# Performance work log

Hardware: AMD Instinct MI355X
Metric: run time of the kernel (lower is better)

## Reference

```python
import jax, jax.numpy as jnp
import numpy as np

B, T, V, H, L = 4, 2048, 32000, 512, 2

def setup_inputs() -> dict:
    key = jax.random.key(0)
    ks = jax.random.split(key, 8)
    s = 0.04  # ~1/sqrt(H) scaling to keep tanh unsaturated
    return {
        "x": jax.random.randint(ks[0], (B, T), 0, V, dtype=jnp.int32),
        "embed": jax.random.normal(ks[1], (V, H), jnp.float32) * s,
        "W_ih": jax.random.normal(ks[2], (L, H, H), jnp.float32) * s,
        "b_ih": jax.random.normal(ks[3], (L, H), jnp.float32) * s,
        "W_hh": jax.random.normal(ks[4], (L, H, H), jnp.float32) * s,
        "b_hh": jax.random.normal(ks[5], (L, H), jnp.float32) * s,
        "W_out": jax.random.normal(ks[6], (V, H), jnp.float32) * s,
        "b_out": jax.random.normal(ks[7], (V,), jnp.float32) * s,
    }

def reference(x, embed, W_ih, b_ih, W_hh, b_hh, W_out, b_out):
    emb = embed[x]                      # [B, T, H]
    num_layers = W_ih.shape[0]
    Bsz = x.shape[0]
    Hd = embed.shape[1]

    def step(h, x_t):                   # h: [L, B, H], x_t: [B, H]
        inp = x_t
        new_h = []
        for l in range(num_layers):     # small fixed layer count
            hl = jnp.tanh(inp @ W_ih[l].T + b_ih[l] + h[l] @ W_hh[l].T + b_hh[l])
            new_h.append(hl)
            inp = hl
        out = inp @ W_out.T + b_out     # [B, V]
        return jnp.stack(new_h), out

    h0 = jnp.zeros((num_layers, Bsz, Hd), emb.dtype)
    h_final, outs = jax.lax.scan(step, h0, jnp.swapaxes(emb, 0, 1))  # outs: [T, B, V]
    return jnp.swapaxes(outs, 0, 1), h_final
```

## Files before the change

### kernel.cpp

```cpp
#include <hip/hip_runtime.h>
#include <stdint.h>

#define Bdim 4
#define Tdim 2048
#define Vdim 32000
#define Hdim 512
#define MROWS (Bdim * Tdim)

typedef unsigned short u16;
typedef __bf16 bf16x8 __attribute__((ext_vector_type(8)));
typedef float f32x4 __attribute__((ext_vector_type(4)));

__device__ __forceinline__ u16 f2bf(float f) {
  union { float f; uint32_t u; } a; a.f = f;
  uint32_t r = a.u + 0x7FFFu + ((a.u >> 16) & 1u);
  return (u16)(r >> 16);
}

__global__ void k_gather(const int* __restrict__ x, const float* __restrict__ embed,
                         u16* __restrict__ E) {
  int idx = blockIdx.x * 256 + threadIdx.x;
  int row = idx >> 7;
  int c4  = (idx & 127) << 2;
  int tok = x[row];
  const float4 v = *(const float4*)(embed + (size_t)tok * Hdim + c4);
  *(ushort4*)(E + (size_t)row * Hdim + c4) =
      make_ushort4(f2bf(v.x), f2bf(v.y), f2bf(v.z), f2bf(v.w));
}

__global__ void k_f2b(const float* __restrict__ in, u16* __restrict__ out, int n4) {
  int idx = blockIdx.x * 256 + threadIdx.x;
  if (idx >= n4) return;
  const float4 v = *(const float4*)(in + (size_t)idx * 4);
  *(ushort4*)(out + (size_t)idx * 4) =
      make_ushort4(f2bf(v.x), f2bf(v.y), f2bf(v.z), f2bf(v.w));
}

__device__ __forceinline__ void g2l16(const void* g, void* l) {
  __builtin_amdgcn_global_load_lds(
      (const __attribute__((address_space(1))) uint32_t*)g,
      (__attribute__((address_space(3))) uint32_t*)l, 16, 0, 0);
}

__global__ __launch_bounds__(256, 2) void k_gemm(
    const u16* __restrict__ A, const u16* __restrict__ Bw, float* __restrict__ C,
    const float* __restrict__ bias1, const float* __restrict__ bias2,
    int M, int N, int K, int ntN)
{
  __shared__ u16 Al[128 * 64];
  __shared__ u16 Bl[128 * 64];
  const int bid = blockIdx.x;
  const int mt = bid / ntN, nt = bid % ntN;
  const int m0 = mt << 7, n0 = nt << 7;
  const int tid = threadIdx.x;
  const int l = tid & 63, w = tid >> 6;
  const int wy = w >> 1, wx = w & 1;
  const int frow = l & 15, fk = (l >> 4) << 3;

  f32x4 acc[4][4];
  #pragma unroll
  for (int a = 0; a < 4; ++a)
    #pragma unroll
    for (int b = 0; b < 4; ++b) acc[a][b] = f32x4{0.f, 0.f, 0.f, 0.f};

  for (int kb = 0; kb < K; kb += 64) {
    __syncthreads();
    #pragma unroll
    for (int is = 0; is < 4; ++is) {
      const int off = tid * 16 + is * 4096;
      const int lrow = off >> 7, lcolB = off & 127;
      g2l16(A  + (size_t)(m0 + lrow) * K + kb + (lcolB >> 1), (char*)Al + off);
      g2l16(Bw + (size_t)(n0 + lrow) * K + kb + (lcolB >> 1), (char*)Bl + off);
    }
    __syncthreads();
    #pragma unroll
    for (int ks = 0; ks < 2; ++ks) {
      bf16x8 af[4], bfr[4];
      #pragma unroll
      for (int mi = 0; mi < 4; ++mi)
        af[mi] = *(const bf16x8*)&Al[((wy * 64 + mi * 16 + frow) << 6) + ks * 32 + fk];
      #pragma unroll
      for (int ni = 0; ni < 4; ++ni)
        bfr[ni] = *(const bf16x8*)&Bl[((wx * 64 + ni * 16 + frow) << 6) + ks * 32 + fk];
      #pragma unroll
      for (int mi = 0; mi < 4; ++mi)
        #pragma unroll
        for (int ni = 0; ni < 4; ++ni)
          acc[mi][ni] = __builtin_amdgcn_mfma_f32_16x16x32_bf16(af[mi], bfr[ni], acc[mi][ni], 0, 0, 0);
    }
  }
  #pragma unroll
  for (int ni = 0; ni < 4; ++ni) {
    const int col = n0 + wx * 64 + ni * 16 + (l & 15);
    float bv = bias1[col];
    if (bias2) bv += bias2[col];
    #pragma unroll
    for (int mi = 0; mi < 4; ++mi) {
      const int row = m0 + wy * 64 + mi * 16 + ((l >> 4) << 2);
      #pragma unroll
      for (int r = 0; r < 4; ++r)
        C[(size_t)(row + r) * N + col] = acc[mi][ni][r] + bv;
    }
  }
}

#define SENT 0xFFFFFFFFu

__device__ __forceinline__ uint64_t al64(const uint64_t* p) {
  return __hip_atomic_load(p, __ATOMIC_RELAXED, __HIP_MEMORY_SCOPE_AGENT);
}
__device__ __forceinline__ void astore(uint32_t* p, uint32_t v) {
  __hip_atomic_store(p, v, __ATOMIC_RELAXED, __HIP_MEMORY_SCOPE_AGENT);
}
__device__ __forceinline__ bool bad2(uint64_t x) {
  return ((uint32_t)x == SENT) || ((uint32_t)(x >> 32) == SENT);
}
#define SPIN2(va, vb, P)                                          \
  while (bad2(va) || bad2(vb)) {                                  \
    if (bad2(va)) va = al64(P);                                   \
    if (bad2(vb)) vb = al64((P) + 1);                             \
  }

#define ROWDW 264

template <bool IS_L1>
__device__ __forceinline__ void scan_wg(
    const float* __restrict__ X0,
    const float* __restrict__ W1,
    const float* __restrict__ W2,
    const float* __restrict__ bi1, const float* __restrict__ bi2,
    uint32_t* __restrict__ H0b, uint32_t* __restrict__ H1b,
    float* __restrict__ hfin, int wgs, uint32_t* hsA, uint32_t* hsB)
{
  constexpr int NB = IS_L1 ? 32 : 16;
  const int tid = threadIdx.x;
  const int wv  = tid >> 6;
  const int l   = tid & 63;
  const int n   = l & 15;
  const int cq  = l >> 4;
  const int ng  = wgs * 64 + wv * 16 + n;
  const int fb  = n & 3;
  const int pb  = wv;
  const int q   = l;

  bf16x8 bw[NB];
  #pragma unroll
  for (int j = 0; j < NB; ++j) {
    const float* wrow;
    int koff;
    if constexpr (IS_L1) {
      if (j < 16) { wrow = W1 + (size_t)ng * Hdim; koff = j * 32; }
      else        { wrow = W2 + (size_t)ng * Hdim; koff = (j - 16) * 32; }
    } else        { wrow = W1 + (size_t)ng * Hdim; koff = j * 32; }
    const float4 a = *(const float4*)(wrow + koff + cq * 8);
    const float4 b = *(const float4*)(wrow + koff + cq * 8 + 4);
    bw[j][0] = (__bf16)a.x; bw[j][1] = (__bf16)a.y;
    bw[j][2] = (__bf16)a.z; bw[j][3] = (__bf16)a.w;
    bw[j][4] = (__bf16)b.x; bw[j][5] = (__bf16)b.y;
    bw[j][6] = (__bf16)b.z; bw[j][7] = (__bf16)b.w;
  }
  float bias = 0.f;
  if constexpr (IS_L1) bias = bi1[ng] + bi2[ng];

  const uint64_t *PpA = nullptr, *PpB = nullptr;
  uint64_t vaA = 0, vbA = 0, vaB = 0, vbB = 0;
  if constexpr (IS_L1) {
    PpA = (const uint64_t*)(H0b + ((size_t)pb * Tdim + 0) * 256 + 4 * q);
    vaA = al64(PpA); vbA = al64(PpA + 1);
  }

  #pragma unroll 1
  for (int t = 0; t < Tdim; ++t) {
    uint32_t* sA = hsA + (t & 1) * (4 * ROWDW);
    f32x4 ac[4];
    #pragma unroll
    for (int x = 0; x < 4; ++x) ac[x] = f32x4{0.f, 0.f, 0.f, 0.f};

    if constexpr (!IS_L1) {
      float x0v[4];
      #pragma unroll
      for (int r = 0; r < 4; ++r)
        x0v[r] = X0[((size_t)r * Tdim + t) * Hdim + ng];

      if (t > 0) {
        SPIN2(vaA, vbA, PpA);
        uint4 u;
        u.x = (uint32_t)vaA; u.y = (uint32_t)(vaA >> 32);
        u.z = (uint32_t)vbA; u.w = (uint32_t)(vbA >> 32);
        *(uint4*)(sA + pb * ROWDW + 4 * q) = u;
      }
      PpA = (const uint64_t*)(H0b + ((size_t)pb * Tdim + t) * 256 + 4 * q);
      vaA = al64(PpA); vbA = al64(PpA + 1);

      if (t > 0) {
        __syncthreads();
        const u16* sA16 = (const u16*)sA;
        #pragma unroll
        for (int j = 0; j < 16; ++j) {
          const bf16x8 af = *(const bf16x8*)&sA16[fb * (2 * ROWDW) + j * 32 + cq * 8];
          ac[j & 3] = __builtin_amdgcn_mfma_f32_16x16x32_bf16(af, bw[j], ac[j & 3], 0, 0, 0);
        }
      }
      const f32x4 s = (ac[0] + ac[1]) + (ac[2] + ac[3]);
      float hv[4], hp[4];
      #pragma unroll
      for (int r = 0; r < 4; ++r) hv[r] = tanhf(s[r] + x0v[r]);
      #pragma unroll
      for (int r = 0; r < 4; ++r) hp[r] = __shfl_xor(hv[r], 1);
      if (cq == 0) {
        if (!(n & 1)) {
          #pragma unroll
          for (int r = 0; r < 4; ++r) {
            const uint32_t wd = (uint32_t)f2bf(hv[r]) | ((uint32_t)f2bf(hp[r]) << 16);
            astore(&H0b[((size_t)r * Tdim + t) * 256 + (ng >> 1)], wd);
          }
        }
        if (t == Tdim - 1) {
          #pragma unroll
          for (int r = 0; r < 4; ++r) hfin[r * Hdim + ng] = hv[r];
        }
      }
    } else {
      uint32_t* sB = hsB + (t & 1) * (4 * ROWDW);
      if (t > 0) {
        SPIN2(vaB, vbB, PpB);
        uint4 u;
        u.x = (uint32_t)vaB; u.y = (uint32_t)(vaB >> 32);
        u.z = (uint32_t)vbB; u.w = (uint32_t)(vbB >> 32);
        *(uint4*)(sB + pb * ROWDW + 4 * q) = u;
        __syncthreads();
        const u16* sB16 = (const u16*)sB;
        #pragma unroll
        for (int j = 16; j < 32; ++j) {
          const bf16x8 af = *(const bf16x8*)&sB16[fb * (2 * ROWDW) + (j - 16) * 32 + cq * 8];
          ac[j & 3] = __builtin_amdgcn_mfma_f32_16x16x32_bf16(af, bw[j], ac[j & 3], 0, 0, 0);
        }
      }
      SPIN2(vaA, vbA, PpA);
      {
        uint4 u;
        u.x = (uint32_t)vaA; u.y = (uint32_t)(vaA >> 32);
        u.z = (uint32_t)vbA; u.w = (uint32_t)(vbA >> 32);
        *(uint4*)(sA + pb * ROWDW + 4 * q) = u;
      }
      {
        const int tn = (t + 1 < Tdim) ? t + 1 : t;
        PpA = (const uint64_t*)(H0b + ((size_t)pb * Tdim + tn) * 256 + 4 * q);
        vaA = al64(PpA); vbA = al64(PpA + 1);
      }
      __syncthreads();
      const u16* sA16 = (const u16*)sA;
      #pragma unroll
      for (int j = 0; j < 16; ++j) {
        const bf16x8 af = *(const bf16x8*)&sA16[fb * (2 * ROWDW) + j * 32 + cq * 8];
        ac[j & 3] = __builtin_amdgcn_mfma_f32_16x16x32_bf16(af, bw[j], ac[j & 3], 0, 0, 0);
      }
      const f32x4 s = (ac[0] + ac[1]) + (ac[2] + ac[3]);
      float hv[4], hp[4];
      #pragma unroll
      for (int r = 0; r < 4; ++r) hv[r] = tanhf(s[r] + bias);
      #pragma unroll
      for (int r = 0; r < 4; ++r) hp[r] = __shfl_xor(hv[r], 1);
      if (cq == 0) {
        if (!(n & 1)) {
          #pragma unroll
          for (int r = 0; r < 4; ++r) {
            const uint32_t wd = (uint32_t)f2bf(hv[r]) | ((uint32_t)f2bf(hp[r]) << 16);
            astore(&H1b[((size_t)r * Tdim + t) * 256 + (ng >> 1)], wd);
          }
        }
        if (t == Tdim - 1) {
          #pragma unroll
          for (int r = 0; r < 4; ++r) hfin[Bdim * Hdim + r * Hdim + ng] = hv[r];
        }
      }
      PpB = (const uint64_t*)(H1b + ((size_t)pb * Tdim + t) * 256 + 4 * q);
      vaB = al64(PpB); vbB = al64(PpB + 1);
    }
  }
}

__global__ __launch_bounds__(256, 1) void k_scan(
    const float* __restrict__ X0, const float* __restrict__ W_ih,
    const float* __restrict__ W_hh, const float* __restrict__ b_ih,
    const float* __restrict__ b_hh, uint32_t* __restrict__ H0b,
    uint32_t* __restrict__ H1b, float* __restrict__ hfin)
{
  __shared__ __align__(16) uint32_t hsA[2 * 4 * ROWDW];
  __shared__ __align__(16) uint32_t hsB[2 * 4 * ROWDW];
  const int blk = blockIdx.x;
  if (blk < 8)
    scan_wg<false>(X0, W_hh, nullptr, nullptr, nullptr, H0b, H1b, hfin, blk, hsA, hsB);
  else
    scan_wg<true>(nullptr, W_ih + Hdim * Hdim, W_hh + Hdim * Hdim,
                  b_ih + Hdim, b_hh + Hdim, H0b, H1b, hfin, blk - 8, hsA, hsB);
}

extern "C" void kernel_launch(void* const* d_in, const int* in_sizes, int n_in,
                              void* d_out, int out_size, void* d_ws, size_t ws_size,
                              hipStream_t stream)
{
  const int*   x     = (const int*)d_in[0];
  const float* embed = (const float*)d_in[1];
  const float* W_ih  = (const float*)d_in[2];
  const float* b_ih  = (const float*)d_in[3];
  const float* W_hh  = (const float*)d_in[4];
  const float* b_hh  = (const float*)d_in[5];
  const float* W_out = (const float*)d_in[6];
  const float* b_out = (const float*)d_in[7];
  float* out = (float*)d_out;

  char* ws = (char*)d_ws;
  u16* E       = (u16*)ws;
  u16* Wih0b   = E + (size_t)MROWS * Hdim;
  u16* Woutb   = Wih0b + Hdim * Hdim;
  float* X0    = (float*)(Woutb + (size_t)Vdim * Hdim);
  uint32_t* H0b = (uint32_t*)(X0 + (size_t)MROWS * Hdim);
  uint32_t* H1b = H0b + (size_t)MROWS * (Hdim / 2);

  k_gather<<<MROWS * (Hdim / 4) / 256, 256, 0, stream>>>(x, embed, E);
  k_f2b<<<(Hdim * Hdim / 4) / 256, 256, 0, stream>>>(W_ih, Wih0b, Hdim * Hdim / 4);
  k_f2b<<<(Vdim * Hdim / 4) / 256, 256, 0, stream>>>(W_out, Woutb, Vdim * Hdim / 4);

  k_gemm<<<(MROWS / 128) * (Hdim / 128), 256, 0, stream>>>(
      E, Wih0b, X0, b_ih, b_hh, MROWS, Hdim, Hdim, Hdim / 128);

  hipMemsetAsync(H0b, 0xFF, (size_t)MROWS * (Hdim / 2) * 4, stream);
  hipMemsetAsync(H1b, 0xFF, (size_t)MROWS * (Hdim / 2) * 4, stream);

  float* hfin = out + (size_t)MROWS * Vdim;
  k_scan<<<16, 256, 0, stream>>>(X0, W_ih, W_hh, b_ih, b_hh, H0b, H1b, hfin);

  k_gemm<<<(MROWS / 128) * (Vdim / 128), 256, 0, stream>>>(
      (const u16*)H1b, Woutb, out, b_out, nullptr, MROWS, Vdim, Hdim, Vdim / 128);
}
```

Baseline: 6.846 ms.

## Replace block-wide barrier with per-wave polling and staging in recurrent scan

Each wave now polls the whole previous hidden-state row itself, using wide cache-bypassing dwordx4 loads, and stages it into its own private LDS region, so the per-step __syncthreads is gone. Layer 1 issues its layer-0 load early and overlaps it with the recurrent MFMA work. Layer 0 is throttled so it stays no more than 128 steps ahead of layer 1. The scan grid grows to 128 blocks with only every eighth block active, which appears meant to spread the 16 workers across different XCDs or CUs. The cost is redundant global polling by every wave, plus reliance on inline asm ordering and cache-modifier semantics.

```diff
diff --git a/kernel.cpp b/kernel.cpp
--- a/kernel.cpp
+++ b/kernel.cpp
@@ -10,6 +10,7 @@
 typedef unsigned short u16;
 typedef __bf16 bf16x8 __attribute__((ext_vector_type(8)));
 typedef float f32x4 __attribute__((ext_vector_type(4)));
+typedef uint32_t u32x4 __attribute__((ext_vector_type(4)));
 
 __device__ __forceinline__ u16 f2bf(float f) {
   union { float f; uint32_t u; } a; a.f = f;
@@ -106,22 +107,96 @@
 
 #define SENT 0xFFFFFFFFu
 
-__device__ __forceinline__ uint64_t al64(const uint64_t* p) {
-  return __hip_atomic_load(p, __ATOMIC_RELAXED, __HIP_MEMORY_SCOPE_AGENT);
-}
 __device__ __forceinline__ void astore(uint32_t* p, uint32_t v) {
   __hip_atomic_store(p, v, __ATOMIC_RELAXED, __HIP_MEMORY_SCOPE_AGENT);
 }
-__device__ __forceinline__ bool bad2(uint64_t x) {
-  return ((uint32_t)x == SENT) || ((uint32_t)(x >> 32) == SENT);
-}
-#define SPIN2(va, vb, P)                                          \
-  while (bad2(va) || bad2(vb)) {                                  \
-    if (bad2(va)) va = al64(P);                                   \
-    if (bad2(vb)) vb = al64((P) + 1);                             \
-  }
-
-#define ROWDW 264
+__device__ __forceinline__ uint32_t aload(const uint32_t* p) {
+  return __hip_atomic_load(p, __ATOMIC_RELAXED, __HIP_MEMORY_SCOPE_AGENT);
+}
+
+__device__ __forceinline__ void pollload(const uint32_t* p, u32x4& a, u32x4& b,
+                                         u32x4& c, u32x4& d) {
+  asm volatile(
+      "global_load_dwordx4 %0, %4, off sc0\n\t"
+      "global_load_dwordx4 %1, %4, off offset:16 sc0\n\t"
+      "global_load_dwordx4 %2, %4, off offset:32 sc0\n\t"
+      "global_load_dwordx4 %3, %4, off offset:48 sc0\n\t"
+      "s_waitcnt vmcnt(0)"
+      : "=&v"(a), "=&v"(b), "=&v"(c), "=&v"(d)
+      : "v"(p) : "memory");
+  __builtin_amdgcn_sched_barrier(0);
+}
+__device__ __forceinline__ void pissue(const uint32_t* p, u32x4& a, u32x4& b,
+                                       u32x4& c, u32x4& d) {
+  asm volatile(
+      "global_load_dwordx4 %0, %4, off sc0\n\t"
+      "global_load_dwordx4 %1, %4, off offset:16 sc0\n\t"
+      "global_load_dwordx4 %2, %4, off offset:32 sc0\n\t"
+      "global_load_dwordx4 %3, %4, off offset:48 sc0"
+      : "=&v"(a), "=&v"(b), "=&v"(c), "=&v"(d)
+      : "v"(p) : "memory");
+}
+__device__ __forceinline__ void pwait(u32x4& a, u32x4& b, u32x4& c, u32x4& d) {
+  asm volatile("s_waitcnt vmcnt(0)"
+               : "+v"(a), "+v"(b), "+v"(c), "+v"(d) :: "memory");
+  __builtin_amdgcn_sched_barrier(0);
+}
+__device__ __forceinline__ bool any_sent(const u32x4& a, const u32x4& b,
+                                         const u32x4& c, const u32x4& d) {
+  bool bad = false;
+  #pragma unroll
+  for (int j = 0; j < 4; ++j)
+    bad |= (a[j] == SENT) | (b[j] == SENT) | (c[j] == SENT) | (d[j] == SENT);
+  return bad;
+}
+__device__ __forceinline__ void respin(const uint32_t* p, u32x4& a, u32x4& b,
+                                       u32x4& c, u32x4& d) {
+  int tr = 0;
+  while (any_sent(a, b, c, d)) {
+    if (tr < 2) {
+      pollload(p, a, b, c, d);
+    } else {
+      #pragma unroll
+      for (int j = 0; j < 4; ++j) {
+        if (a[j] == SENT) a[j] = aload(p + j);
+        if (b[j] == SENT) b[j] = aload(p + 4 + j);
+        if (c[j] == SENT) c[j] = aload(p + 8 + j);
+        if (d[j] == SENT) d[j] = aload(p + 12 + j);
+      }
+    }
+    ++tr;
+  }
+}
+__device__ __forceinline__ void spin16(const uint32_t* p, u32x4& a, u32x4& b,
+                                       u32x4& c, u32x4& d) {
+  pollload(p, a, b, c, d);
+  respin(p, a, b, c, d);
+}
+__device__ __forceinline__ void spin_word(const uint32_t* p) {
+  uint32_t v;
+  asm volatile("global_load_dword %0, %1, off sc0\n\ts_waitcnt vmcnt(0)"
+               : "=&v"(v) : "v"(p) : "memory");
+  __builtin_amdgcn_sched_barrier(0);
+  int tr = 0;
+  while (v == SENT) {
+    if (tr < 2)
+      asm volatile("global_load_dword %0, %1, off sc0\n\ts_waitcnt vmcnt(0)"
+                   : "=&v"(v) : "v"(p) : "memory");
+    else
+      v = aload(p);
+    ++tr;
+  }
+  __builtin_amdgcn_sched_barrier(0);
+}
+__device__ __forceinline__ void lds_guard() {
+  asm volatile("s_waitcnt lgkmcnt(0)" ::: "memory");
+  __builtin_amdgcn_sched_barrier(0);
+}
+
+#define STAGE(base, A, B, C, D) do {                      \
+    uint32_t* _d = (base) + sb * 264 + sq * 16;           \
+    *(u32x4*)(_d)      = (A); *(u32x4*)(_d + 4)  = (B);   \
+    *(u32x4*)(_d + 8)  = (C); *(u32x4*)(_d + 12) = (D); } while (0)
 
 template <bool IS_L1>
 __device__ __forceinline__ void scan_wg(
@@ -130,7 +205,7 @@
     const float* __restrict__ W2,
     const float* __restrict__ bi1, const float* __restrict__ bi2,
     uint32_t* __restrict__ H0b, uint32_t* __restrict__ H1b,
-    float* __restrict__ hfin, int wgs, uint32_t* hsA, uint32_t* hsB)
+    float* __restrict__ hfin, int wgs, uint32_t* hs)
 {
   constexpr int NB = IS_L1 ? 32 : 16;
   const int tid = threadIdx.x;
@@ -140,8 +215,13 @@
   const int cq  = l >> 4;
   const int ng  = wgs * 64 + wv * 16 + n;
   const int fb  = n & 3;
-  const int pb  = wv;
-  const int q   = l;
+  const int sb  = l >> 4;
+  const int sq  = l & 15;
+
+  uint32_t* hsA = hs + wv * 1056;
+  uint32_t* hsB = hs + 4224 + wv * 1056;
+  const u16* sA16 = (const u16*)hsA;
+  const u16* sB16 = (const u16*)hsB;
 
   bf16x8 bw[NB];
   #pragma unroll
@@ -162,120 +242,90 @@
   float bias = 0.f;
   if constexpr (IS_L1) bias = bi1[ng] + bi2[ng];
 
-  const uint64_t *PpA = nullptr, *PpB = nullptr;
-  uint64_t vaA = 0, vbA = 0, vaB = 0, vbB = 0;
-  if constexpr (IS_L1) {
-    PpA = (const uint64_t*)(H0b + ((size_t)pb * Tdim + 0) * 256 + 4 * q);
-    vaA = al64(PpA); vbA = al64(PpA + 1);
-  }
+  uint32_t* const Hout = IS_L1 ? H1b : H0b;
 
   #pragma unroll 1
   for (int t = 0; t < Tdim; ++t) {
-    uint32_t* sA = hsA + (t & 1) * (4 * ROWDW);
     f32x4 ac[4];
     #pragma unroll
-    for (int x = 0; x < 4; ++x) ac[x] = f32x4{0.f, 0.f, 0.f, 0.f};
+    for (int q = 0; q < 4; ++q) ac[q] = f32x4{0.f, 0.f, 0.f, 0.f};
+    float hv[4], hp[4];
 
     if constexpr (!IS_L1) {
+      u32x4 a, b, c, d;
+      if (t > 0)
+        spin16(H0b + ((size_t)sb * Tdim + (t - 1)) * 256 + sq * 16, a, b, c, d);
       float x0v[4];
       #pragma unroll
       for (int r = 0; r < 4; ++r)
         x0v[r] = X0[((size_t)r * Tdim + t) * Hdim + ng];
-
       if (t > 0) {
-        SPIN2(vaA, vbA, PpA);
-        uint4 u;
-        u.x = (uint32_t)vaA; u.y = (uint32_t)(vaA >> 32);
-        u.z = (uint32_t)vbA; u.w = (uint32_t)(vbA >> 32);
-        *(uint4*)(sA + pb * ROWDW + 4 * q) = u;
-      }
-      PpA = (const uint64_t*)(H0b + ((size_t)pb * Tdim + t) * 256 + 4 * q);
-      vaA = al64(PpA); vbA = al64(PpA + 1);
-
-      if (t > 0) {
-        __syncthreads();
-        const u16* sA16 = (const u16*)sA;
+        lds_guard();
+        STAGE(hsA, a, b, c, d);
         #pragma unroll
         for (int j = 0; j < 16; ++j) {
-          const bf16x8 af = *(const bf16x8*)&sA16[fb * (2 * ROWDW) + j * 32 + cq * 8];
+          const bf16x8 af = *(const bf16x8*)&sA16[fb * 528 + j * 32 + cq * 8];
           ac[j & 3] = __builtin_amdgcn_mfma_f32_16x16x32_bf16(af, bw[j], ac[j & 3], 0, 0, 0);
         }
       }
       const f32x4 s = (ac[0] + ac[1]) + (ac[2] + ac[3]);
-      float hv[4], hp[4];
       #pragma unroll
       for (int r = 0; r < 4; ++r) hv[r] = tanhf(s[r] + x0v[r]);
       #pragma unroll
       for (int r = 0; r < 4; ++r) hp[r] = __shfl_xor(hv[r], 1);
-      if (cq == 0) {
-        if (!(n & 1)) {
-          #pragma unroll
-          for (int r = 0; r < 4; ++r) {
-            const uint32_t wd = (uint32_t)f2bf(hv[r]) | ((uint32_t)f2bf(hp[r]) << 16);
-            astore(&H0b[((size_t)r * Tdim + t) * 256 + (ng >> 1)], wd);
-          }
+      if (cq == 0 && !(n & 1)) {
+        #pragma unroll
+        for (int r = 0; r < 4; ++r) {
+          const uint32_t wd = (uint32_t)f2bf(hv[r]) | ((uint32_t)f2bf(hp[r]) << 16);
+          astore(&Hout[((size_t)r * Tdim + t) * 256 + (ng >> 1)], wd);
         }
-        if (t == Tdim - 1) {
-          #pragma unroll
-          for (int r = 0; r < 4; ++r) hfin[r * Hdim + ng] = hv[r];
+      }
+      if (cq == 0 && t == Tdim - 1) {
+        #pragma unroll
+        for (int r = 0; r < 4; ++r) hfin[r * Hdim + ng] = hv[r];
+      }
+      if (t >= 128 && (t & 15) == 0)
+        spin_word(H1b + (size_t)(t - 128) * 256);
+    } else {
+      u32x4 a, b, c, d, e, f, g, h2;
+      if (t > 0) {
+        spin16(H1b + ((size_t)sb * Tdim + (t - 1)) * 256 + sq * 16, e, f, g, h2);
+        lds_guard();
+        STAGE(hsB, e, f, g, h2);
+        pissue(H0b + ((size_t)sb * Tdim + t) * 256 + sq * 16, a, b, c, d);
+        #pragma unroll
+        for (int j = 0; j < 16; ++j) {
+          const bf16x8 af = *(const bf16x8*)&sB16[fb * 528 + j * 32 + cq * 8];
+          ac[j & 3] = __builtin_amdgcn_mfma_f32_16x16x32_bf16(af, bw[16 + j], ac[j & 3], 0, 0, 0);
         }
-      }
-    } else {
-      uint32_t* sB = hsB + (t & 1) * (4 * ROWDW);
-      if (t > 0) {
-        SPIN2(vaB, vbB, PpB);
-        uint4 u;
-        u.x = (uint32_t)vaB; u.y = (uint32_t)(vaB >> 32);
-        u.z = (uint32_t)vbB; u.w = (uint32_t)(vbB >> 32);
-        *(uint4*)(sB + pb * ROWDW + 4 * q) = u;
-        __syncthreads();
-        const u16* sB16 = (const u16*)sB;
-        #pragma unroll
-        for (int j = 16; j < 32; ++j) {
-          const bf16x8 af = *(const bf16x8*)&sB16[fb * (2 * ROWDW) + (j - 16) * 32 + cq * 8];
-          ac[j & 3] = __builtin_amdgcn_mfma_f32_16x16x32_bf16(af, bw[j], ac[j & 3], 0, 0, 0);
+        pwait(a, b, c, d);
+        respin(H0b + ((size_t)sb * Tdim + t) * 256 + sq * 16, a, b, c, d);
+      } else {
+        spin16(H0b + ((size_t)sb * Tdim + 0) * 256 + sq * 16, a, b, c, d);
+      }
+      lds_guard();
+      STAGE(hsA, a, b, c, d);
+      #pragma unroll
+      for (int j = 0; j < 16; ++j) {
+        const bf16x8 af = *(const bf16x8*)&sA16[fb * 528 + j * 32 + cq * 8];
+        ac[j & 3] = __builtin_amdgcn_mfma_f32_16x16x32_bf16(af, bw[j], ac[j & 3], 0, 0, 0);
+      }
+      const f32x4 s = (ac[0] + ac[1]) + (ac[2] + ac[3]);
+      #pragma unroll
+      for (int r = 0; r < 4; ++r) hv[r] = tanhf(s[r] + bias);
+      #pragma unroll
+      for (int r = 0; r < 4; ++r) hp[r] = __shfl_xor(hv[r], 1);
+      if (cq == 0 && !(n & 1)) {
+        #pragma unroll
+        for (int r = 0; r < 4; ++r) {
+          const uint32_t wd = (uint32_t)f2bf(hv[r]) | ((uint32_t)f2bf(hp[r]) << 16);
+          astore(&Hout[((size_t)r * Tdim + t) * 256 + (ng >> 1)], wd);
         }
       }
-      SPIN2(vaA, vbA, PpA);
-      {
-        uint4 u;
-        u.x = (uint32_t)vaA; u.y = (uint32_t)(vaA >> 32);
-        u.z = (uint32_t)vbA; u.w = (uint32_t)(vbA >> 32);
-        *(uint4*)(sA + pb * ROWDW + 4 * q) = u;
-      }
-      {
-        const int tn = (t + 1 < Tdim) ? t + 1 : t;
-        PpA = (const uint64_t*)(H0b + ((size_t)pb * Tdim + tn) * 256 + 4 * q);
-        vaA = al64(PpA); vbA = al64(PpA + 1);
-      }
-      __syncthreads();
-      const u16* sA16 = (const u16*)sA;
-      #pragma unroll
-      for (int j = 0; j < 16; ++j) {
-        const bf16x8 af = *(const bf16x8*)&sA16[fb * (2 * ROWDW) + j * 32 + cq * 8];
-        ac[j & 3] = __builtin_amdgcn_mfma_f32_16x16x32_bf16(af, bw[j], ac[j & 3], 0, 0, 0);
-      }
-      const f32x4 s = (ac[0] + ac[1]) + (ac[2] + ac[3]);
-      float hv[4], hp[4];
-      #pragma unroll
-      for (int r = 0; r < 4; ++r) hv[r] = tanhf(s[r] + bias);
-      #pragma unroll
-      for (int r = 0; r < 4; ++r) hp[r] = __shfl_xor(hv[r], 1);
-      if (cq == 0) {
-        if (!(n & 1)) {
-          #pragma unroll
-          for (int r = 0; r < 4; ++r) {
-            const uint32_t wd = (uint32_t)f2bf(hv[r]) | ((uint32_t)f2bf(hp[r]) << 16);
-            astore(&H1b[((size_t)r * Tdim + t) * 256 + (ng >> 1)], wd);
-          }
-        }
-        if (t == Tdim - 1) {
-          #pragma unroll
-          for (int r = 0; r < 4; ++r) hfin[Bdim * Hdim + r * Hdim + ng] = hv[r];
-        }
-      }
-      PpB = (const uint64_t*)(H1b + ((size_t)pb * Tdim + t) * 256 + 4 * q);
-      vaB = al64(PpB); vbB = al64(PpB + 1);
+      if (cq == 0 && t == Tdim - 1) {
+        #pragma unroll
+        for (int r = 0; r < 4; ++r) hfin[Bdim * Hdim + r * Hdim + ng] = hv[r];
+      }
     }
   }
 }
@@ -286,14 +336,14 @@
     const float* __restrict__ b_hh, uint32_t* __restrict__ H0b,
     uint32_t* __restrict__ H1b, float* __restrict__ hfin)
 {
-  __shared__ __align__(16) uint32_t hsA[2 * 4 * ROWDW];
-  __shared__ __align__(16) uint32_t hsB[2 * 4 * ROWDW];
-  const int blk = blockIdx.x;
-  if (blk < 8)
-    scan_wg<false>(X0, W_hh, nullptr, nullptr, nullptr, H0b, H1b, hfin, blk, hsA, hsB);
+  __shared__ __align__(16) uint32_t hs[8448];
+  if (blockIdx.x & 7) return;
+  const int wg = blockIdx.x >> 3;
+  if (wg < 8)
+    scan_wg<false>(X0, W_hh, nullptr, nullptr, nullptr, H0b, H1b, hfin, wg, hs);
   else
     scan_wg<true>(nullptr, W_ih + Hdim * Hdim, W_hh + Hdim * Hdim,
-                  b_ih + Hdim, b_hh + Hdim, H0b, H1b, hfin, blk - 8, hsA, hsB);
+                  b_ih + Hdim, b_hh + Hdim, H0b, H1b, hfin, wg - 8, hs);
 }
 
 extern "C" void kernel_launch(void* const* d_in, const int* in_sizes, int n_in,
@@ -329,7 +379,7 @@
   hipMemsetAsync(H1b, 0xFF, (size_t)MROWS * (Hdim / 2) * 4, stream);
 
   float* hfin = out + (size_t)MROWS * Vdim;
-  k_scan<<<16, 256, 0, stream>>>(X0, W_ih, W_hh, b_ih, b_hh, H0b, H1b, hfin);
+  k_scan<<<128, 256, 0, stream>>>(X0, W_ih, W_hh, b_ih, b_hh, H0b, H1b, hfin);
 
   k_gemm<<<(MROWS / 128) * (Vdim / 128), 256, 0, stream>>>(
       (const u16*)H1b, Woutb, out, b_out, nullptr, MROWS, Vdim, Hdim, Vdim / 128);
```

Result: slower. 12.04 ms (+75.8%).
